# Optimization experiments

Hardware: AMD Instinct MI355X
Metric: run time of the kernel (lower is better)

The kernel has to match this reference:

```python
import jax, jax.numpy as jnp
import numpy as np

N = 50000          # nodes
L = 8              # tokens per node (EmbeddingBag bag size)
E = 800000         # graph edges
N_EDGE_TYPES = 4
NODE_DIM = 256
TOKEN_DIM = 128
TYPE_DIM = 64
ANNOT_DIM = 192
MSG_DIM = 128
N_TOKENS = 100000
N_TYPES = 200


def setup_inputs() -> dict:
    key = jax.random.key(0)
    ks = jax.random.split(key, 16)
    inp = {
        "var_type": jax.random.randint(ks[0], (N,), 0, N_TYPES),
        "node_tokens": jax.random.randint(ks[1], (N, L), 0, N_TOKENS),
        "mask": jax.random.uniform(ks[2], (N, L), dtype=jnp.float32),
        "adj_rows": jax.random.randint(ks[3], (E,), 0, N),
        "adj_cols": jax.random.randint(ks[4], (E,), 0, N * N_EDGE_TYPES),
        "adj_vals": jnp.ones((E,), dtype=jnp.float32),
        "n_steps": 5,
        # learned parameters
        "tok_emb": jax.random.normal(ks[5], (N_TOKENS, TOKEN_DIM), jnp.float32) * 0.02,
        "type_emb": jax.random.normal(ks[6], (N_TYPES, TYPE_DIM), jnp.float32) * 0.02,
        "sg_w": jax.random.normal(ks[7], (TOKEN_DIM + TYPE_DIM, ANNOT_DIM), jnp.float32) * 0.02,
        "sg_b": jnp.zeros((ANNOT_DIM,), jnp.float32),
        "msg_w": jax.random.normal(ks[8], (NODE_DIM, MSG_DIM * N_EDGE_TYPES), jnp.float32) * 0.02,
        "msg_b": jnp.zeros((MSG_DIM * N_EDGE_TYPES,), jnp.float32),
        "w_ih": jax.random.normal(ks[9], (3 * NODE_DIM, MSG_DIM), jnp.float32) * 0.02,
        "w_hh": jax.random.normal(ks[10], (3 * NODE_DIM, NODE_DIM), jnp.float32) * 0.02,
        "b_ih": jnp.zeros((3 * NODE_DIM,), jnp.float32),
        "b_hh": jnp.zeros((3 * NODE_DIM,), jnp.float32),
    }
    return inp


def _gru_cell(x, h, w_ih, w_hh, b_ih, b_hh):
    # torch nn.GRUCell math
    gi = x @ w_ih.T + b_ih          # [N, 3H]
    gh = h @ w_hh.T + b_hh          # [N, 3H]
    i_r, i_z, i_n = jnp.split(gi, 3, axis=1)
    h_r, h_z, h_n = jnp.split(gh, 3, axis=1)
    r = jax.nn.sigmoid(i_r + h_r)
    z = jax.nn.sigmoid(i_z + h_z)
    n = jnp.tanh(i_n + r * h_n)
    return (1.0 - z) * n + z * h


def reference(var_type, node_tokens, mask, adj_rows, adj_cols, adj_vals, n_steps,
              tok_emb, type_emb, sg_w, sg_b, msg_w, msg_b, w_ih, w_hh, b_ih, b_hh):
    # EmbeddingBag(mode='sum', per_sample_weights=mask): [N, token_dim]
    tokens = jnp.sum(tok_emb[node_tokens] * mask[:, :, None], axis=1)
    types = type_emb[var_type]                               # [N, type_dim]
    ann = jnp.concatenate([tokens, types], axis=1) @ sg_w + sg_b   # [N, annot]
    state = jnp.pad(ann, ((0, 0), (0, NODE_DIM - ANNOT_DIM)))      # [N, node_dim]

    # divider = clamp_min(row-sum of sparse adjacency, 1)
    divider = jnp.maximum(
        jax.ops.segment_sum(adj_vals, adj_rows, num_segments=N), 1.0)[:, None]

    def step(st, _):
        msg_out = (st @ msg_w + msg_b).reshape(-1, MSG_DIM)   # [N*n_edges, msg]
        # sparse.mm(adjacency, msg_out): gather source messages, scatter-add to rows
        gathered = msg_out[adj_cols] * adj_vals[:, None]      # [E, msg]
        msg_in = jax.ops.segment_sum(gathered, adj_rows, num_segments=N) / divider
        return _gru_cell(msg_in, st, w_ih, w_hh, b_ih, b_hh), None

    state, _ = jax.lax.scan(step, state, None, length=n_steps)
    return state
```

## Files before the change

kernel.cpp:

```cpp
#include <hip/hip_runtime.h>
#include <hip/hip_bf16.h>


#define N_   50000
#define L_   8
#define E_   800000
#define ND_  256
#define TD_  128
#define TYD_ 64
#define AD_  192
#define MD_  128
#define STEPS_ 5

typedef __attribute__((ext_vector_type(8))) __bf16 bf16x8;
typedef __attribute__((ext_vector_type(4))) float  f32x4;

__global__ __launch_bounds__(256) void k_hist(const int* __restrict__ rows,
                                              const float* __restrict__ vals,
                                              int* __restrict__ cnt,
                                              float* __restrict__ divider, int e_total) {
    int e = blockIdx.x * 256 + threadIdx.x;
    if (e >= e_total) return;
    int r = rows[e];
    atomicAdd(&cnt[r], 1);
    atomicAdd(&divider[r], vals[e]);
}

__global__ __launch_bounds__(1024) void k_scan(const int* __restrict__ cnt,
                                               int* __restrict__ row_start, int n) {
    __shared__ int s[1024];
    __shared__ int carry_s;
    int tid = threadIdx.x;
    if (tid == 0) carry_s = 0;
    __syncthreads();
    for (int base = 0; base < n; base += 1024) {
        int x = (base + tid < n) ? cnt[base + tid] : 0;
        s[tid] = x;
        __syncthreads();
        for (int off = 1; off < 1024; off <<= 1) {
            int t = (tid >= off) ? s[tid - off] : 0;
            __syncthreads();
            s[tid] += t;
            __syncthreads();
        }
        int carry = carry_s;
        if (base + tid < n) row_start[base + tid] = carry + s[tid] - x;
        __syncthreads();
        if (tid == 1023) carry_s = carry + s[1023];
        __syncthreads();
    }
    if (tid == 0) row_start[n] = carry_s;
}

__global__ __launch_bounds__(256) void k_seed(const int* __restrict__ rs,
                                              int* __restrict__ cursor, int n) {
    int i = blockIdx.x * 256 + threadIdx.x;
    if (i < n) cursor[i] = rs[i];
}

__global__ __launch_bounds__(256) void k_scatter(const int* __restrict__ rows,
                                                 const int* __restrict__ cols,
                                                 const float* __restrict__ vals,
                                                 int* __restrict__ cursor,
                                                 int* __restrict__ edst,
                                                 float* __restrict__ ew, int e_total) {
    int e = blockIdx.x * 256 + threadIdx.x;
    if (e >= e_total) return;
    int r = rows[e];
    int p = atomicAdd(&cursor[r], 1);
    edst[p] = cols[e];
    ew[p]   = vals[e];
}

__global__ __launch_bounds__(256) void k_wsplit_d(const float* __restrict__ src,
                                                  __bf16* __restrict__ hi,
                                                  __bf16* __restrict__ lo, int total) {
    int t = blockIdx.x * 256 + threadIdx.x;
    if (t >= total) return;
    float w = src[t];
    __bf16 h = (__bf16)w;
    hi[t] = h;
    lo[t] = (__bf16)(w - (float)h);
}

__global__ __launch_bounds__(256) void k_wsplit_t(const float* __restrict__ src,
                                                  __bf16* __restrict__ hi,
                                                  __bf16* __restrict__ lo, int K, int J) {
    int t = blockIdx.x * 256 + threadIdx.x;
    if (t >= K * J) return;
    int j = t / K, k = t - j * K;
    float w = src[(size_t)k * J + j];
    __bf16 h = (__bf16)w;
    hi[t] = h;
    lo[t] = (__bf16)(w - (float)h);
}

__global__ __launch_bounds__(256) void k_embed(const int* __restrict__ node_tokens,
                                               const float* __restrict__ mask,
                                               const int* __restrict__ var_type,
                                               const float* __restrict__ tok_emb,
                                               const float* __restrict__ type_emb,
                                               float* __restrict__ annot_in) {
    int t = blockIdx.x * 256 + threadIdx.x;
    if (t >= N_ * AD_) return;
    int n = t / AD_, d = t - n * AD_;
    float v;
    if (d < TD_) {
        v = 0.f;
#pragma unroll
        for (int l = 0; l < L_; l++) {
            int idx = node_tokens[n * L_ + l];
            v += tok_emb[idx * TD_ + d] * mask[n * L_ + l];
        }
    } else {
        v = type_emb[var_type[n] * TYD_ + (d - TD_)];
    }
    annot_in[t] = v;
}

__global__ __launch_bounds__(256) void k_gemm_mfma(
        const float* __restrict__ A, int lda,
        const __bf16* __restrict__ Whi, const __bf16* __restrict__ Wlo,
        const float* __restrict__ bias,
        float* __restrict__ OUT, int ldout,
        int M, int K, int J) {
    __shared__ __align__(16) __bf16 sAhi[64 * 32];
    __shared__ __align__(16) __bf16 sAlo[64 * 32];
    __shared__ __align__(16) __bf16 sWhi[128 * 32];
    __shared__ __align__(16) __bf16 sWlo[128 * 32];

    int tid  = threadIdx.x;
    int m0   = blockIdx.x * 64;
    int j0   = blockIdx.y * 128;
    int lane = tid & 63;
    int wv   = tid >> 6;
    int wm   = (wv >> 1) * 32;
    int wn   = (wv & 1) * 64;
    int l15  = lane & 15;
    int lg   = lane >> 4;
    int sl   = lg ^ (l15 & 3);

    int ar  = tid >> 2, akg = tid & 3;
    int aoff = ar * 32 + (akg ^ (ar & 3)) * 8;
    const float* asrc = A + (size_t)(m0 + ar) * lda + akg * 8;
    bool arow_ok = (m0 + ar) < M;

    int wj = tid >> 1;
    bool wrow_ok = (j0 + wj) < J;
    size_t wbase = (size_t)(j0 + wj) * K;

    f32x4 acc[2][4];
#pragma unroll
    for (int mi = 0; mi < 2; mi++)
#pragma unroll
        for (int nf = 0; nf < 4; nf++) {
            acc[mi][nf][0] = 0.f; acc[mi][nf][1] = 0.f;
            acc[mi][nf][2] = 0.f; acc[mi][nf][3] = 0.f;
        }

    for (int kk = 0; kk < K; kk += 32) {
        {
            float v[8];
            if (arow_ok) {
                float4 p0 = *(const float4*)(asrc + kk);
                float4 p1 = *(const float4*)(asrc + kk + 4);
                v[0] = p0.x; v[1] = p0.y; v[2] = p0.z; v[3] = p0.w;
                v[4] = p1.x; v[5] = p1.y; v[6] = p1.z; v[7] = p1.w;
            } else {
#pragma unroll
                for (int q = 0; q < 8; q++) v[q] = 0.f;
            }
            bf16x8 hiv, lov;
#pragma unroll
            for (int q = 0; q < 8; q++) {
                __bf16 h = (__bf16)v[q];
                hiv[q] = h;
                lov[q] = (__bf16)(v[q] - (float)h);
            }
            *(bf16x8*)&sAhi[aoff] = hiv;
            *(bf16x8*)&sAlo[aoff] = lov;
        }
#pragma unroll
        for (int h = 0; h < 2; h++) {
            int kg   = (tid & 1) * 2 + h;
            int off  = wj * 32 + (kg ^ (wj & 3)) * 8;
            bf16x8 hv, lv;
            if (wrow_ok) {
                hv = *(const bf16x8*)(Whi + wbase + kk + kg * 8);
                lv = *(const bf16x8*)(Wlo + wbase + kk + kg * 8);
            } else {
#pragma unroll
                for (int q = 0; q < 8; q++) { hv[q] = (__bf16)0.f; lv[q] = (__bf16)0.f; }
            }
            *(bf16x8*)&sWhi[off] = hv;
            *(bf16x8*)&sWlo[off] = lv;
        }
        __syncthreads();
        bf16x8 ah[2], al[2], bh[4], bl[4];
#pragma unroll
        for (int mi = 0; mi < 2; mi++) {
            int idx = (wm + mi * 16 + l15) * 32 + sl * 8;
            ah[mi] = *(bf16x8*)&sAhi[idx];
            al[mi] = *(bf16x8*)&sAlo[idx];
        }
#pragma unroll
        for (int nf = 0; nf < 4; nf++) {
            int idx = (wn + nf * 16 + l15) * 32 + sl * 8;
            bh[nf] = *(bf16x8*)&sWhi[idx];
            bl[nf] = *(bf16x8*)&sWlo[idx];
        }
#pragma unroll
        for (int mi = 0; mi < 2; mi++)
#pragma unroll
            for (int nf = 0; nf < 4; nf++) {
                acc[mi][nf] = __builtin_amdgcn_mfma_f32_16x16x32_bf16(ah[mi], bh[nf], acc[mi][nf], 0, 0, 0);
                acc[mi][nf] = __builtin_amdgcn_mfma_f32_16x16x32_bf16(al[mi], bh[nf], acc[mi][nf], 0, 0, 0);
                acc[mi][nf] = __builtin_amdgcn_mfma_f32_16x16x32_bf16(ah[mi], bl[nf], acc[mi][nf], 0, 0, 0);
            }
        __syncthreads();
    }
#pragma unroll
    for (int mi = 0; mi < 2; mi++) {
        int gmb = m0 + wm + mi * 16 + lg * 4;
#pragma unroll
        for (int nf = 0; nf < 4; nf++) {
            int gj = j0 + wn + nf * 16 + l15;
            if (gj >= J) continue;
            float bs = bias[gj];
#pragma unroll
            for (int r2 = 0; r2 < 4; r2++) {
                int gm = gmb + r2;
                if (gm < M) OUT[(size_t)gm * ldout + gj] = acc[mi][nf][r2] + bs;
            }
        }
    }
}

__global__ __launch_bounds__(128) void k_edge(const int* __restrict__ row_start,
                                              const int* __restrict__ edge_dst,
                                              const float* __restrict__ edge_w,
                                              const float* __restrict__ msg_out,
                                              const float* __restrict__ divider,
                                              float* __restrict__ msg_in) {
    int n = blockIdx.x;
    int d = threadIdx.x;
    int s = row_start[n], e = row_start[n + 1];
    float acc = 0.f;
    for (int i = s; i < e; i++) {
        int c = edge_dst[i];
        float v = edge_w[i];
        acc += msg_out[(size_t)c * MD_ + d] * v;
    }
    float dv = divider[n];
    dv = dv < 1.f ? 1.f : dv;
    msg_in[(size_t)n * MD_ + d] = acc / dv;
}

__global__ __launch_bounds__(256) void k_gru_elem(const float* __restrict__ gi,
                                                  const float* __restrict__ gh,
                                                  const float* __restrict__ st_in,
                                                  float* __restrict__ st_out, int M) {
    int t = blockIdx.x * 256 + threadIdx.x;
    if (t >= M * ND_) return;
    int n = t >> 8, h = t & 255;
    const float* gir = gi + (size_t)n * 768;
    const float* ghr = gh + (size_t)n * 768;
    float i_r = gir[h], i_z = gir[256 + h], i_n = gir[512 + h];
    float h_r = ghr[h], h_z = ghr[256 + h], h_n = ghr[512 + h];
    float r = 1.f / (1.f + expf(-(i_r + h_r)));
    float z = 1.f / (1.f + expf(-(i_z + h_z)));
    float nn = tanhf(i_n + r * h_n);
    float hp = st_in[t];
    st_out[t] = (1.f - z) * nn + z * hp;
}

extern "C" void kernel_launch(void* const* d_in, const int* in_sizes, int n_in,
                              void* d_out, int out_size, void* d_ws, size_t ws_size,
                              hipStream_t stream) {
    const int*   var_type    = (const int*)  d_in[0];
    const int*   node_tokens = (const int*)  d_in[1];
    const float* mask        = (const float*)d_in[2];
    const int*   adj_rows    = (const int*)  d_in[3];
    const int*   adj_cols    = (const int*)  d_in[4];
    const float* adj_vals    = (const float*)d_in[5];
    const float* tok_emb     = (const float*)d_in[7];
    const float* type_emb    = (const float*)d_in[8];
    const float* sg_w        = (const float*)d_in[9];
    const float* sg_b        = (const float*)d_in[10];
    const float* msg_w       = (const float*)d_in[11];
    const float* msg_b       = (const float*)d_in[12];
    const float* w_ih        = (const float*)d_in[13];
    const float* w_hh        = (const float*)d_in[14];
    const float* b_ih        = (const float*)d_in[15];
    const float* b_hh        = (const float*)d_in[16];
    float* out = (float*)d_out;

    float* f = (float*)d_ws;
    float* state0   = f;        f += (size_t)N_ * 256;
    float* msg_out  = f;        f += (size_t)N_ * 512;
    float* msg_in   = f;        f += (size_t)N_ * 128;
    float* divider  = f;        f += N_;
    int*   row_start= (int*)f;  f += N_ + 4;
    int*   cursor   = (int*)f;  f += N_;
    int*   edge_dst = (int*)f;  f += E_;
    float* edge_w   = f;        f += E_;
    __bf16* sgw_hi  = (__bf16*)f;
    __bf16* sgw_lo  = sgw_hi + 192 * 192;
    __bf16* msgw_hi = sgw_lo + 192 * 192;
    __bf16* msgw_lo = msgw_hi + 512 * 256;
    __bf16* wih_hi  = msgw_lo + 512 * 256;
    __bf16* wih_lo  = wih_hi + 768 * 128;
    __bf16* whh_hi  = wih_lo + 768 * 128;
    __bf16* whh_lo  = whh_hi + 768 * 256;

    hipMemsetAsync(divider, 0, (size_t)(N_ + (N_ + 4) + N_) * sizeof(float), stream);
    hipMemsetAsync(state0, 0, (size_t)N_ * 256 * sizeof(float), stream);

    k_hist<<<(E_ + 255) / 256, 256, 0, stream>>>(adj_rows, adj_vals, cursor, divider, E_);
    k_scan<<<1, 1024, 0, stream>>>(cursor, row_start, N_);
    k_seed<<<(N_ + 255) / 256, 256, 0, stream>>>(row_start, cursor, N_);
    k_scatter<<<(E_ + 255) / 256, 256, 0, stream>>>(adj_rows, adj_cols, adj_vals,
                                                    cursor, edge_dst, edge_w, E_);
    k_wsplit_t<<<(192 * 192 + 255) / 256, 256, 0, stream>>>(sg_w, sgw_hi, sgw_lo, 192, 192);
    k_wsplit_t<<<(256 * 512 + 255) / 256, 256, 0, stream>>>(msg_w, msgw_hi, msgw_lo, 256, 512);
    k_wsplit_d<<<(768 * 128 + 255) / 256, 256, 0, stream>>>(w_ih, wih_hi, wih_lo, 768 * 128);
    k_wsplit_d<<<(768 * 256 + 255) / 256, 256, 0, stream>>>(w_hh, whh_hi, whh_lo, 768 * 256);

    float* annot_in = msg_out;
    k_embed<<<(N_ * AD_ + 255) / 256, 256, 0, stream>>>(node_tokens, mask, var_type,
                                                        tok_emb, type_emb, annot_in);
    {
        dim3 g((N_ + 63) / 64, 2);
        k_gemm_mfma<<<g, 256, 0, stream>>>(annot_in, AD_, sgw_hi, sgw_lo, sg_b,
                                           state0, 256, N_, AD_, AD_);
    }

    for (int s = 0; s < STEPS_; s++) {
        float* cur = (s & 1) ? out : state0;
        float* nxt = (s & 1) ? state0 : out;

        {
            dim3 g((N_ + 63) / 64, 4);
            k_gemm_mfma<<<g, 256, 0, stream>>>(cur, 256, msgw_hi, msgw_lo, msg_b,
                                               msg_out, 512, N_, 256, 512);
        }
        k_edge<<<N_, 128, 0, stream>>>(row_start, edge_dst, edge_w, msg_out, divider, msg_in);

        for (int c = 0; c < 4; c++) {
            int c0 = c * 12500;
            const int Mc = 12500;
            float* gi = msg_out;
            float* gh = msg_out + (size_t)12500 * 768;
            dim3 g((Mc + 63) / 64, 6);
            k_gemm_mfma<<<g, 256, 0, stream>>>(msg_in + (size_t)c0 * 128, 128,
                                               wih_hi, wih_lo, b_ih, gi, 768, Mc, 128, 768);
            k_gemm_mfma<<<g, 256, 0, stream>>>(cur + (size_t)c0 * 256, 256,
                                               whh_hi, whh_lo, b_hh, gh, 768, Mc, 256, 768);
            k_gru_elem<<<(Mc * 256 + 255) / 256, 256, 0, stream>>>(
                gi, gh, cur + (size_t)c0 * 256, nxt + (size_t)c0 * 256, Mc);
        }
    }
}
```

Baseline: 2.910 ms.

## Keep activations pre-split as bf16 hi/lo and load GEMM tiles directly into LDS

```diff
diff --git a/kernel.cpp b/kernel.cpp
--- a/kernel.cpp
+++ b/kernel.cpp
@@ -14,6 +14,12 @@
 
 typedef __attribute__((ext_vector_type(8))) __bf16 bf16x8;
 typedef __attribute__((ext_vector_type(4))) float  f32x4;
+
+__device__ __forceinline__ void gl_lds16(const void* g, void* l) {
+    __builtin_amdgcn_global_load_lds(
+        (const __attribute__((address_space(1))) void*)g,
+        (__attribute__((address_space(3))) void*)l, 16, 0, 0);
+}
 
 __global__ __launch_bounds__(256) void k_hist(const int* __restrict__ rows,
                                               const float* __restrict__ vals,
@@ -100,7 +106,8 @@
                                                const int* __restrict__ var_type,
                                                const float* __restrict__ tok_emb,
                                                const float* __restrict__ type_emb,
-                                               float* __restrict__ annot_in) {
+                                               __bf16* __restrict__ ann_hi,
+                                               __bf16* __restrict__ ann_lo) {
     int t = blockIdx.x * 256 + threadIdx.x;
     if (t >= N_ * AD_) return;
     int n = t / AD_, d = t - n * AD_;
@@ -115,43 +122,54 @@
     } else {
         v = type_emb[var_type[n] * TYD_ + (d - TD_)];
     }
-    annot_in[t] = v;
-}
-
-__global__ __launch_bounds__(256) void k_gemm_mfma(
-        const float* __restrict__ A, int lda,
+    __bf16 h = (__bf16)v;
+    ann_hi[t] = h;
+    ann_lo[t] = (__bf16)(v - (float)h);
+}
+
+template<int MODE>
+__global__ __launch_bounds__(256) void k_gemm_bf16(
+        const __bf16* __restrict__ Ahi, const __bf16* __restrict__ Alo,
         const __bf16* __restrict__ Whi, const __bf16* __restrict__ Wlo,
         const float* __restrict__ bias,
-        float* __restrict__ OUT, int ldout,
-        int M, int K, int J) {
-    __shared__ __align__(16) __bf16 sAhi[64 * 32];
-    __shared__ __align__(16) __bf16 sAlo[64 * 32];
-    __shared__ __align__(16) __bf16 sWhi[128 * 32];
-    __shared__ __align__(16) __bf16 sWlo[128 * 32];
-
-    int tid  = threadIdx.x;
-    int m0   = blockIdx.x * 64;
-    int j0   = blockIdx.y * 128;
-    int lane = tid & 63;
-    int wv   = tid >> 6;
-    int wm   = (wv >> 1) * 32;
-    int wn   = (wv & 1) * 64;
-    int l15  = lane & 15;
-    int lg   = lane >> 4;
-    int sl   = lg ^ (l15 & 3);
-
-    int ar  = tid >> 2, akg = tid & 3;
-    int aoff = ar * 32 + (akg ^ (ar & 3)) * 8;
-    const float* asrc = A + (size_t)(m0 + ar) * lda + akg * 8;
-    bool arow_ok = (m0 + ar) < M;
-
-    int wj = tid >> 1;
-    bool wrow_ok = (j0 + wj) < J;
-    size_t wbase = (size_t)(j0 + wj) * K;
-
-    f32x4 acc[2][4];
-#pragma unroll
-    for (int mi = 0; mi < 2; mi++)
+        float* __restrict__ OUT,
+        __bf16* __restrict__ OUThi, __bf16* __restrict__ OUTlo,
+        int ldout, int M, int K, int J) {
+    __shared__ __align__(16) __bf16 sAh[4096];
+    __shared__ __align__(16) __bf16 sAl[4096];
+    __shared__ __align__(16) __bf16 sWh[4096];
+    __shared__ __align__(16) __bf16 sWl[4096];
+
+    const int tid  = threadIdx.x;
+    const int lane = tid & 63;
+    const int wv   = tid >> 6;
+    const int wm   = (wv >> 1) * 64;
+    const int wn   = (wv & 1) * 64;
+    const int l15  = lane & 15;
+    const int lg   = lane >> 4;
+    const int m0   = blockIdx.x * 128;
+    const int j0   = blockIdx.y * 128;
+
+    const int ar0 = min(m0 + lane,      M - 1);
+    const int ar1 = min(m0 + 64 + lane, M - 1);
+    const int wr0 = min(j0 + lane,      J - 1);
+    const int wr1 = min(j0 + 64 + lane, J - 1);
+    const size_t aoff0 = (size_t)ar0 * K + wv * 8;
+    const size_t aoff1 = (size_t)ar1 * K + wv * 8;
+    const size_t woff0 = (size_t)wr0 * K + wv * 8;
+    const size_t woff1 = (size_t)wr1 * K + wv * 8;
+    __bf16* dA0 = &sAh[wv * 1024];
+    __bf16* dA1 = &sAh[wv * 1024 + 512];
+    __bf16* dB0 = &sAl[wv * 1024];
+    __bf16* dB1 = &sAl[wv * 1024 + 512];
+    __bf16* dC0 = &sWh[wv * 1024];
+    __bf16* dC1 = &sWh[wv * 1024 + 512];
+    __bf16* dD0 = &sWl[wv * 1024];
+    __bf16* dD1 = &sWl[wv * 1024 + 512];
+
+    f32x4 acc[4][4];
+#pragma unroll
+    for (int mi = 0; mi < 4; mi++)
 #pragma unroll
         for (int nf = 0; nf < 4; nf++) {
             acc[mi][nf][0] = 0.f; acc[mi][nf][1] = 0.f;
@@ -159,58 +177,31 @@
         }
 
     for (int kk = 0; kk < K; kk += 32) {
-        {
-            float v[8];
-            if (arow_ok) {
-                float4 p0 = *(const float4*)(asrc + kk);
-                float4 p1 = *(const float4*)(asrc + kk + 4);
-                v[0] = p0.x; v[1] = p0.y; v[2] = p0.z; v[3] = p0.w;
-                v[4] = p1.x; v[5] = p1.y; v[6] = p1.z; v[7] = p1.w;
-            } else {
-#pragma unroll
-                for (int q = 0; q < 8; q++) v[q] = 0.f;
-            }
-            bf16x8 hiv, lov;
-#pragma unroll
-            for (int q = 0; q < 8; q++) {
-                __bf16 h = (__bf16)v[q];
-                hiv[q] = h;
-                lov[q] = (__bf16)(v[q] - (float)h);
-            }
-            *(bf16x8*)&sAhi[aoff] = hiv;
-            *(bf16x8*)&sAlo[aoff] = lov;
-        }
-#pragma unroll
-        for (int h = 0; h < 2; h++) {
-            int kg   = (tid & 1) * 2 + h;
-            int off  = wj * 32 + (kg ^ (wj & 3)) * 8;
-            bf16x8 hv, lv;
-            if (wrow_ok) {
-                hv = *(const bf16x8*)(Whi + wbase + kk + kg * 8);
-                lv = *(const bf16x8*)(Wlo + wbase + kk + kg * 8);
-            } else {
-#pragma unroll
-                for (int q = 0; q < 8; q++) { hv[q] = (__bf16)0.f; lv[q] = (__bf16)0.f; }
-            }
-            *(bf16x8*)&sWhi[off] = hv;
-            *(bf16x8*)&sWlo[off] = lv;
-        }
+        gl_lds16(Ahi + aoff0 + kk, dA0);
+        gl_lds16(Ahi + aoff1 + kk, dA1);
+        gl_lds16(Alo + aoff0 + kk, dB0);
+        gl_lds16(Alo + aoff1 + kk, dB1);
+        gl_lds16(Whi + woff0 + kk, dC0);
+        gl_lds16(Whi + woff1 + kk, dC1);
+        gl_lds16(Wlo + woff0 + kk, dD0);
+        gl_lds16(Wlo + woff1 + kk, dD1);
         __syncthreads();
-        bf16x8 ah[2], al[2], bh[4], bl[4];
-#pragma unroll
-        for (int mi = 0; mi < 2; mi++) {
-            int idx = (wm + mi * 16 + l15) * 32 + sl * 8;
-            ah[mi] = *(bf16x8*)&sAhi[idx];
-            al[mi] = *(bf16x8*)&sAlo[idx];
+
+        bf16x8 ah[4], al[4], bh[4], bl[4];
+#pragma unroll
+        for (int mi = 0; mi < 4; mi++) {
+            int idx = (lg * 128 + wm + mi * 16 + l15) * 8;
+            ah[mi] = *(bf16x8*)&sAh[idx];
+            al[mi] = *(bf16x8*)&sAl[idx];
         }
 #pragma unroll
         for (int nf = 0; nf < 4; nf++) {
-            int idx = (wn + nf * 16 + l15) * 32 + sl * 8;
-            bh[nf] = *(bf16x8*)&sWhi[idx];
-            bl[nf] = *(bf16x8*)&sWlo[idx];
-        }
-#pragma unroll
-        for (int mi = 0; mi < 2; mi++)
+            int idx = (lg * 128 + wn + nf * 16 + l15) * 8;
+            bh[nf] = *(bf16x8*)&sWh[idx];
+            bl[nf] = *(bf16x8*)&sWl[idx];
+        }
+#pragma unroll
+        for (int mi = 0; mi < 4; mi++)
 #pragma unroll
             for (int nf = 0; nf < 4; nf++) {
                 acc[mi][nf] = __builtin_amdgcn_mfma_f32_16x16x32_bf16(ah[mi], bh[nf], acc[mi][nf], 0, 0, 0);
@@ -220,7 +211,7 @@
         __syncthreads();
     }
 #pragma unroll
-    for (int mi = 0; mi < 2; mi++) {
+    for (int mi = 0; mi < 4; mi++) {
         int gmb = m0 + wm + mi * 16 + lg * 4;
 #pragma unroll
         for (int nf = 0; nf < 4; nf++) {
@@ -230,7 +221,15 @@
 #pragma unroll
             for (int r2 = 0; r2 < 4; r2++) {
                 int gm = gmb + r2;
-                if (gm < M) OUT[(size_t)gm * ldout + gj] = acc[mi][nf][r2] + bs;
+                if (gm >= M) continue;
+                float v = acc[mi][nf][r2] + bs;
+                if constexpr (MODE == 0) {
+                    OUT[(size_t)gm * ldout + gj] = v;
+                } else {
+                    __bf16 h = (__bf16)v;
+                    OUThi[(size_t)gm * ldout + gj] = h;
+                    OUTlo[(size_t)gm * ldout + gj] = (__bf16)(v - (float)h);
+                }
             }
         }
     }
@@ -241,28 +240,45 @@
                                               const float* __restrict__ edge_w,
                                               const float* __restrict__ msg_out,
                                               const float* __restrict__ divider,
-                                              float* __restrict__ msg_in) {
+                                              __bf16* __restrict__ min_hi,
+                                              __bf16* __restrict__ min_lo) {
     int n = blockIdx.x;
     int d = threadIdx.x;
     int s = row_start[n], e = row_start[n + 1];
     float acc = 0.f;
-    for (int i = s; i < e; i++) {
+    int i = s;
+    for (; i + 3 < e; i += 4) {
+        int   c0 = edge_dst[i],   c1 = edge_dst[i+1], c2 = edge_dst[i+2], c3 = edge_dst[i+3];
+        float w0 = edge_w[i],     w1 = edge_w[i+1],   w2 = edge_w[i+2],   w3 = edge_w[i+3];
+        float m0v = msg_out[(size_t)c0 * MD_ + d];
+        float m1v = msg_out[(size_t)c1 * MD_ + d];
+        float m2v = msg_out[(size_t)c2 * MD_ + d];
+        float m3v = msg_out[(size_t)c3 * MD_ + d];
+        acc += m0v * w0 + m1v * w1 + m2v * w2 + m3v * w3;
+    }
+    for (; i < e; i++) {
         int c = edge_dst[i];
-        float v = edge_w[i];
-        acc += msg_out[(size_t)c * MD_ + d] * v;
+        acc += msg_out[(size_t)c * MD_ + d] * edge_w[i];
     }
     float dv = divider[n];
     dv = dv < 1.f ? 1.f : dv;
-    msg_in[(size_t)n * MD_ + d] = acc / dv;
+    float v = acc / dv;
+    __bf16 h = (__bf16)v;
+    min_hi[(size_t)n * MD_ + d] = h;
+    min_lo[(size_t)n * MD_ + d] = (__bf16)(v - (float)h);
 }
 
 __global__ __launch_bounds__(256) void k_gru_elem(const float* __restrict__ gi,
                                                   const float* __restrict__ gh,
-                                                  const float* __restrict__ st_in,
-                                                  float* __restrict__ st_out, int M) {
+                                                  const __bf16* __restrict__ cur_hi,
+                                                  const __bf16* __restrict__ cur_lo,
+                                                  __bf16* __restrict__ nxt_hi,
+                                                  __bf16* __restrict__ nxt_lo,
+                                                  float* __restrict__ outF, int M) {
     int t = blockIdx.x * 256 + threadIdx.x;
     if (t >= M * ND_) return;
-    int n = t >> 8, h = t & 255;
+    int n = t >> 8;
+    int h = t & 255;
     const float* gir = gi + (size_t)n * 768;
     const float* ghr = gh + (size_t)n * 768;
     float i_r = gir[h], i_z = gir[256 + h], i_n = gir[512 + h];
@@ -270,8 +286,15 @@
     float r = 1.f / (1.f + expf(-(i_r + h_r)));
     float z = 1.f / (1.f + expf(-(i_z + h_z)));
     float nn = tanhf(i_n + r * h_n);
-    float hp = st_in[t];
-    st_out[t] = (1.f - z) * nn + z * hp;
+    float hp = (float)cur_hi[t] + (float)cur_lo[t];
+    float st = (1.f - z) * nn + z * hp;
+    if (outF != nullptr) {
+        outF[t] = st;
+    } else {
+        __bf16 sh = (__bf16)st;
+        nxt_hi[t] = sh;
+        nxt_lo[t] = (__bf16)(st - (float)sh);
+    }
 }
 
 extern "C" void kernel_launch(void* const* d_in, const int* in_sizes, int n_in,
@@ -296,9 +319,13 @@
     float* out = (float*)d_out;
 
     float* f = (float*)d_ws;
-    float* state0   = f;        f += (size_t)N_ * 256;
+    __bf16* stA_hi = (__bf16*)f;
+    __bf16* stA_lo = stA_hi + (size_t)N_ * 256;
+    f += (size_t)N_ * 256;
     float* msg_out  = f;        f += (size_t)N_ * 512;
-    float* msg_in   = f;        f += (size_t)N_ * 128;
+    __bf16* min_hi  = (__bf16*)f;
+    __bf16* min_lo  = min_hi + (size_t)N_ * 128;
+    f += (size_t)N_ * 128;
     float* divider  = f;        f += N_;
     int*   row_start= (int*)f;  f += N_ + 4;
     int*   cursor   = (int*)f;  f += N_;
@@ -313,8 +340,14 @@
     __bf16* whh_hi  = wih_lo + 768 * 128;
     __bf16* whh_lo  = whh_hi + 768 * 256;
 
+    __bf16* stB_hi = (__bf16*)d_out;
+    __bf16* stB_lo = stB_hi + (size_t)N_ * 256;
+
+    __bf16* ann_hi = (__bf16*)msg_out;
+    __bf16* ann_lo = ann_hi + (size_t)N_ * AD_;
+
     hipMemsetAsync(divider, 0, (size_t)(N_ + (N_ + 4) + N_) * sizeof(float), stream);
-    hipMemsetAsync(state0, 0, (size_t)N_ * 256 * sizeof(float), stream);
+    hipMemsetAsync(stA_hi, 0, (size_t)N_ * 256 * 2 * sizeof(__bf16), stream);
 
     k_hist<<<(E_ + 255) / 256, 256, 0, stream>>>(adj_rows, adj_vals, cursor, divider, E_);
     k_scan<<<1, 1024, 0, stream>>>(cursor, row_start, N_);
@@ -326,38 +359,48 @@
     k_wsplit_d<<<(768 * 128 + 255) / 256, 256, 0, stream>>>(w_ih, wih_hi, wih_lo, 768 * 128);
     k_wsplit_d<<<(768 * 256 + 255) / 256, 256, 0, stream>>>(w_hh, whh_hi, whh_lo, 768 * 256);
 
-    float* annot_in = msg_out;
     k_embed<<<(N_ * AD_ + 255) / 256, 256, 0, stream>>>(node_tokens, mask, var_type,
-                                                        tok_emb, type_emb, annot_in);
+                                                        tok_emb, type_emb, ann_hi, ann_lo);
     {
-        dim3 g((N_ + 63) / 64, 2);
-        k_gemm_mfma<<<g, 256, 0, stream>>>(annot_in, AD_, sgw_hi, sgw_lo, sg_b,
-                                           state0, 256, N_, AD_, AD_);
+        dim3 g((N_ + 127) / 128, 2);
+        k_gemm_bf16<1><<<g, 256, 0, stream>>>(ann_hi, ann_lo, sgw_hi, sgw_lo, sg_b,
+                                              nullptr, stA_hi, stA_lo, 256, N_, AD_, AD_);
     }
 
     for (int s = 0; s < STEPS_; s++) {
-        float* cur = (s & 1) ? out : state0;
-        float* nxt = (s & 1) ? state0 : out;
+        __bf16* cur_hi = (s & 1) ? stB_hi : stA_hi;
+        __bf16* cur_lo = (s & 1) ? stB_lo : stA_lo;
+        __bf16* nxt_hi = (s & 1) ? stA_hi : stB_hi;
+        __bf16* nxt_lo = (s & 1) ? stA_lo : stB_lo;
+        bool last = (s == STEPS_ - 1);
 
         {
-            dim3 g((N_ + 63) / 64, 4);
-            k_gemm_mfma<<<g, 256, 0, stream>>>(cur, 256, msgw_hi, msgw_lo, msg_b,
-                                               msg_out, 512, N_, 256, 512);
-        }
-        k_edge<<<N_, 128, 0, stream>>>(row_start, edge_dst, edge_w, msg_out, divider, msg_in);
+            dim3 g((N_ + 127) / 128, 4);
+            k_gemm_bf16<0><<<g, 256, 0, stream>>>(cur_hi, cur_lo, msgw_hi, msgw_lo, msg_b,
+                                                  msg_out, nullptr, nullptr, 512, N_, 256, 512);
+        }
+        k_edge<<<N_, 128, 0, stream>>>(row_start, edge_dst, edge_w, msg_out, divider,
+                                       min_hi, min_lo);
 
         for (int c = 0; c < 4; c++) {
-            int c0 = c * 12500;
+            const int c0 = c * 12500;
             const int Mc = 12500;
             float* gi = msg_out;
             float* gh = msg_out + (size_t)12500 * 768;
-            dim3 g((Mc + 63) / 64, 6);
-            k_gemm_mfma<<<g, 256, 0, stream>>>(msg_in + (size_t)c0 * 128, 128,
-                                               wih_hi, wih_lo, b_ih, gi, 768, Mc, 128, 768);
-            k_gemm_mfma<<<g, 256, 0, stream>>>(cur + (size_t)c0 * 256, 256,
-                                               whh_hi, whh_lo, b_hh, gh, 768, Mc, 256, 768);
+            dim3 g((Mc + 127) / 128, 6);
+            k_gemm_bf16<0><<<g, 256, 0, stream>>>(min_hi + (size_t)c0 * 128,
+                                                  min_lo + (size_t)c0 * 128,
+                                                  wih_hi, wih_lo, b_ih,
+                                                  gi, nullptr, nullptr, 768, Mc, 128, 768);
+            k_gemm_bf16<0><<<g, 256, 0, stream>>>(cur_hi + (size_t)c0 * 256,
+                                                  cur_lo + (size_t)c0 * 256,
+                                                  whh_hi, whh_lo, b_hh,
+                                                  gh, nullptr, nullptr, 768, Mc, 256, 768);
             k_gru_elem<<<(Mc * 256 + 255) / 256, 256, 0, stream>>>(
-                gi, gh, cur + (size_t)c0 * 256, nxt + (size_t)c0 * 256, Mc);
-        }
-    }
-}
+                gi, gh,
+                cur_hi + (size_t)c0 * 256, cur_lo + (size_t)c0 * 256,
+                nxt_hi + (size_t)c0 * 256, nxt_lo + (size_t)c0 * 256,
+                last ? (out + (size_t)c0 * 256) : nullptr, Mc);
+        }
+    }
+}
```

Measured after the change: 3.410 ms. 17.2% more time.
